# Performance work log

Hardware: AMD Instinct MI355X
Metric: run time of the kernel (lower is better)

## Reference

```python
import jax, jax.numpy as jnp
import numpy as np

IGNORE_INDEX = 255
LOG_CLAMP = 100.0  # torch BCE clamps log at -100, so -log(x) <= 100


def _neg_log(x, cond):
    # BCE(x, 1) = -log(x), with the torch clamp log(x) >= -100.
    x_safe = jnp.where(cond, jnp.maximum(x, 1e-38), 1.0)
    return jnp.where(cond, jnp.minimum(-jnp.log(x_safe), LOG_CLAMP), 0.0)


def setup_inputs() -> dict:
    key = jax.random.key(0)
    k1, k2 = jax.random.split(key)
    B, C, H, W, D = 1, 20, 256, 256, 32
    pred = jax.random.normal(k1, (B, C, H, W, D), dtype=jnp.float32)
    target = jax.random.randint(k2, (B, H, W, D), 0, C, dtype=jnp.int64)
    return {"pred": pred, "target": target}


def reference(pred, target):
    C = pred.shape[1]
    p = jax.nn.softmax(pred, axis=1)                      # [B,C,H,W,D]
    mask = (target != IGNORE_INDEX)                        # [B,H,W,D]

    # Flatten voxels: [N, C] probs, [N] labels, [N] mask.
    p_flat = jnp.moveaxis(p, 1, -1).reshape(-1, C)
    t_flat = target.reshape(-1)
    m_flat = mask.reshape(-1).astype(p.dtype)
    t_safe = jnp.where(mask.reshape(-1), t_flat, 0).astype(jnp.int32)

    # Per-class reductions in one pass (replaces the per-class python loop):
    # nominator[c] = sum_{masked, t==c} p_c ; ct_count[c] = |{masked, t==c}|
    p_at_t = jnp.take_along_axis(p_flat, t_safe[:, None], axis=1)[:, 0] * m_flat
    nominator = jax.ops.segment_sum(p_at_t, t_safe, num_segments=C)
    ct_count = jax.ops.segment_sum(m_flat, t_safe, num_segments=C)
    sum_p = jnp.einsum('nc,n->c', p_flat, m_flat)          # sum of p_c over masked
    n_masked = jnp.sum(m_flat)

    neg_count = n_masked - ct_count                        # sum(1 - ct)
    spec_num = n_masked - sum_p - ct_count + nominator     # sum((1-p)(1-ct))

    valid = ct_count > 0
    prec = nominator / jnp.maximum(sum_p, 1e-38)
    rec = nominator / jnp.maximum(ct_count, 1.0)
    spec = spec_num / jnp.maximum(neg_count, 1.0)

    loss_c = (_neg_log(prec, valid & (sum_p > 0))
              + _neg_log(rec, valid)
              + _neg_log(spec, valid & (neg_count > 0)))
    count = jnp.sum(valid.astype(p.dtype))
    return jnp.sum(loss_c) / count
```

## Files before the change

### kernel.cpp

```cpp
#include <hip/hip_runtime.h>
#include <math.h>

#define NCLS 20
#define IGNORE_IDX 255
#define LOG2E 1.4426950408889634f
#define NTHR 256
#define NSLOT 32

typedef float v4f __attribute__((ext_vector_type(4)));
typedef int v4i __attribute__((ext_vector_type(4)));

__device__ __forceinline__ float wave_reduce(float v) {
#pragma unroll
  for (int off = 32; off > 0; off >>= 1) v += __shfl_xor(v, off, 64);
  return v;
}

__device__ __forceinline__ float neg_log_clamped(float x, bool cond) {
  if (!cond) return 0.0f;
  float xs = fmaxf(x, 1e-38f);
  return fminf(-logf(xs), 100.0f);
}

__global__ __launch_bounds__(NTHR) void pass1(const float* __restrict__ pred,
                                              const int* __restrict__ target,
                                              float* __restrict__ ws, int N) {
  __shared__ float s_acc[3 * NCLS];
  const int tid = threadIdx.x;
  for (int i = tid; i < 3 * NCLS; i += NTHR) s_acc[i] = 0.0f;
  __syncthreads();

  const int nq = N >> 2;
  const int q = blockIdx.x * NTHR + tid;
  const bool in = (q < nq);

  v4f e[NCLS];
  float w[4] = {0.0f, 0.0f, 0.0f, 0.0f};
  v4f pt = (v4f)(0.0f);
  v4i t4 = {IGNORE_IDX, IGNORE_IDX, IGNORE_IDX, IGNORE_IDX};
#pragma unroll
  for (int c = 0; c < NCLS; ++c) e[c] = (v4f)(0.0f);

  if (in) {
    const int n = q << 2;
    t4 = *reinterpret_cast<const v4i*>(target + n);
    v4f Z = (v4f)(0.0f);
#pragma unroll
    for (int c = 0; c < NCLS; ++c) {
      v4f x = *reinterpret_cast<const v4f*>(pred + (size_t)c * N + n);
#pragma unroll
      for (int j = 0; j < 4; ++j) {
        e[c][j] = __builtin_amdgcn_exp2f(fminf(x[j], 80.0f) * LOG2E);
        Z[j] += e[c][j];
        pt[j] = (c == t4[j]) ? e[c][j] : pt[j];
      }
    }
#pragma unroll
    for (int j = 0; j < 4; ++j) {
      const bool msk = (t4[j] != IGNORE_IDX);
      const float r = __builtin_amdgcn_rcpf(Z[j]);
      w[j] = msk ? r : 0.0f;
    }
  }

#pragma unroll
  for (int c = 0; c < NCLS; ++c) {
    float v = wave_reduce(e[c][0] * w[0] + e[c][1] * w[1] +
                          e[c][2] * w[2] + e[c][3] * w[3]);
    if ((tid & 63) == 0) atomicAdd(&s_acc[c], v);
  }

  if (in) {
#pragma unroll
    for (int j = 0; j < 4; ++j) {
      if (t4[j] != IGNORE_IDX) {
        atomicAdd(&s_acc[NCLS + t4[j]], pt[j] * w[j]);
        atomicAdd(&s_acc[2 * NCLS + t4[j]], 1.0f);
      }
    }
  }
  __syncthreads();

  if (tid < 3 * NCLS)
    atomicAdd(&ws[(size_t)(blockIdx.x & (NSLOT - 1)) * 64 + tid], s_acc[tid]);
}

__global__ __launch_bounds__(64) void pass2(const float* __restrict__ ws,
                                            float* __restrict__ out) {
  __shared__ float s[64];
  const int lane = threadIdx.x;
  float a = 0.0f;
#pragma unroll
  for (int r = 0; r < NSLOT; ++r) a += ws[r * 64 + lane];

  const float n_masked =
      wave_reduce((lane >= 2 * NCLS && lane < 3 * NCLS) ? a : 0.0f);

  s[lane] = a;
  __syncthreads();

  float loss = 0.0f, validf = 0.0f;
  if (lane < NCLS) {
    const float sump = s[lane];
    const float nom = s[NCLS + lane];
    const float cnt = s[2 * NCLS + lane];
    const bool valid = cnt > 0.0f;
    const float prec = nom / fmaxf(sump, 1e-38f);
    const float rec = nom / fmaxf(cnt, 1.0f);
    const float negc = n_masked - cnt;
    const float specn = n_masked - sump - cnt + nom;
    const float spec = specn / fmaxf(negc, 1.0f);
    loss = neg_log_clamped(prec, valid && (sump > 0.0f)) +
           neg_log_clamped(rec, valid) +
           neg_log_clamped(spec, valid && (negc > 0.0f));
    validf = valid ? 1.0f : 0.0f;
  }
  loss = wave_reduce(loss);
  validf = wave_reduce(validf);
  if (lane == 0) out[0] = loss / validf;
}

extern "C" void kernel_launch(void* const* d_in, const int* in_sizes, int n_in,
                              void* d_out, int out_size, void* d_ws, size_t ws_size,
                              hipStream_t stream) {
  const float* pred = (const float*)d_in[0];
  const int* target = (const int*)d_in[1];
  const int N = in_sizes[1];
  const int nq = N >> 2;
  const int nblk = (nq + NTHR - 1) / NTHR;

  hipMemsetAsync(d_ws, 0, NSLOT * 64 * sizeof(float), stream);
  pass1<<<nblk, NTHR, 0, stream>>>(pred, target, (float*)d_ws, N);
  pass2<<<1, 64, 0, stream>>>((const float*)d_ws, (float*)d_out);
}
```

Baseline: 253.8 us.

## Stage pred tile into LDS via direct global-to-LDS async loads

Each block now copies its 20x1024 slice of pred into shared memory with global_load_lds (direct global-to-LDS DMA) before computing, then reads the values back from LDS. The intent is to get many loads in flight at once and cut register pressure from holding 20 vector loads per thread. In exchange each block uses 80KB of LDS, which limits occupancy, and the bounds checks are gone, so N must be a multiple of 1024. The LDS destination offset per wave also relies on the M0/lane addressing working as assumed.

```diff
diff --git a/kernel.cpp b/kernel.cpp
--- a/kernel.cpp
+++ b/kernel.cpp
@@ -1,14 +1,18 @@
 #include <hip/hip_runtime.h>
 #include <math.h>
+#include <stdint.h>
 
 #define NCLS 20
 #define IGNORE_IDX 255
 #define LOG2E 1.4426950408889634f
 #define NTHR 256
+#define VPB 1024
 #define NSLOT 32
 
 typedef float v4f __attribute__((ext_vector_type(4)));
 typedef int v4i __attribute__((ext_vector_type(4)));
+typedef const __attribute__((address_space(1))) uint32_t gu32;
+typedef __attribute__((address_space(3))) uint32_t lu32;
 
 __device__ __forceinline__ float wave_reduce(float v) {
 #pragma unroll
@@ -25,58 +29,60 @@
 __global__ __launch_bounds__(NTHR) void pass1(const float* __restrict__ pred,
                                               const int* __restrict__ target,
                                               float* __restrict__ ws, int N) {
+  __shared__ float s[NCLS * VPB];
   __shared__ float s_acc[3 * NCLS];
   const int tid = threadIdx.x;
+  const int lane = tid & 63;
+  const int w = tid >> 6;
   for (int i = tid; i < 3 * NCLS; i += NTHR) s_acc[i] = 0.0f;
+
+  const int n0 = blockIdx.x * VPB;
+
+#pragma unroll
+  for (int ci = 0; ci < 5; ++ci) {
+    const int c = 5 * w + ci;
+    const float* gbase = pred + (size_t)c * N + n0;
+#pragma unroll
+    for (int k = 0; k < 4; ++k) {
+      __builtin_amdgcn_global_load_lds((gu32*)(gbase + k * 256 + lane * 4),
+                                       (lu32*)&s[c * VPB + k * 256], 16, 0, 0);
+    }
+  }
   __syncthreads();
 
-  const int nq = N >> 2;
-  const int q = blockIdx.x * NTHR + tid;
-  const bool in = (q < nq);
+  const v4i t4 = *reinterpret_cast<const v4i*>(target + n0 + tid * 4);
 
   v4f e[NCLS];
-  float w[4] = {0.0f, 0.0f, 0.0f, 0.0f};
+  v4f Z = (v4f)(0.0f);
   v4f pt = (v4f)(0.0f);
-  v4i t4 = {IGNORE_IDX, IGNORE_IDX, IGNORE_IDX, IGNORE_IDX};
 #pragma unroll
-  for (int c = 0; c < NCLS; ++c) e[c] = (v4f)(0.0f);
-
-  if (in) {
-    const int n = q << 2;
-    t4 = *reinterpret_cast<const v4i*>(target + n);
-    v4f Z = (v4f)(0.0f);
-#pragma unroll
-    for (int c = 0; c < NCLS; ++c) {
-      v4f x = *reinterpret_cast<const v4f*>(pred + (size_t)c * N + n);
-#pragma unroll
-      for (int j = 0; j < 4; ++j) {
-        e[c][j] = __builtin_amdgcn_exp2f(fminf(x[j], 80.0f) * LOG2E);
-        Z[j] += e[c][j];
-        pt[j] = (c == t4[j]) ? e[c][j] : pt[j];
-      }
-    }
+  for (int c = 0; c < NCLS; ++c) {
+    const v4f x = *reinterpret_cast<const v4f*>(&s[c * VPB + tid * 4]);
 #pragma unroll
     for (int j = 0; j < 4; ++j) {
-      const bool msk = (t4[j] != IGNORE_IDX);
-      const float r = __builtin_amdgcn_rcpf(Z[j]);
-      w[j] = msk ? r : 0.0f;
+      e[c][j] = __builtin_amdgcn_exp2f(fminf(x[j], 80.0f) * LOG2E);
+      Z[j] += e[c][j];
+      pt[j] = (c == t4[j]) ? e[c][j] : pt[j];
     }
   }
 
+  float wgt[4];
+#pragma unroll
+  for (int j = 0; j < 4; ++j)
+    wgt[j] = (t4[j] != IGNORE_IDX) ? __builtin_amdgcn_rcpf(Z[j]) : 0.0f;
+
 #pragma unroll
   for (int c = 0; c < NCLS; ++c) {
-    float v = wave_reduce(e[c][0] * w[0] + e[c][1] * w[1] +
-                          e[c][2] * w[2] + e[c][3] * w[3]);
-    if ((tid & 63) == 0) atomicAdd(&s_acc[c], v);
+    const float v = wave_reduce(e[c][0] * wgt[0] + e[c][1] * wgt[1] +
+                                e[c][2] * wgt[2] + e[c][3] * wgt[3]);
+    if (lane == 0) atomicAdd(&s_acc[c], v);
   }
 
-  if (in) {
 #pragma unroll
-    for (int j = 0; j < 4; ++j) {
-      if (t4[j] != IGNORE_IDX) {
-        atomicAdd(&s_acc[NCLS + t4[j]], pt[j] * w[j]);
-        atomicAdd(&s_acc[2 * NCLS + t4[j]], 1.0f);
-      }
+  for (int j = 0; j < 4; ++j) {
+    if (t4[j] != IGNORE_IDX) {
+      atomicAdd(&s_acc[NCLS + t4[j]], pt[j] * wgt[j]);
+      atomicAdd(&s_acc[2 * NCLS + t4[j]], 1.0f);
     }
   }
   __syncthreads();
@@ -126,8 +132,7 @@
   const float* pred = (const float*)d_in[0];
   const int* target = (const int*)d_in[1];
   const int N = in_sizes[1];
-  const int nq = N >> 2;
-  const int nblk = (nq + NTHR - 1) / NTHR;
+  const int nblk = N / VPB;
 
   hipMemsetAsync(d_ws, 0, NSLOT * 64 * sizeof(float), stream);
   pass1<<<nblk, NTHR, 0, stream>>>(pred, target, (float*)d_ws, N);
```

Measured after the change: 294.1 us. 1.16x slower.
